# Optimization experiments

Measured on AMD Instinct MI355X. Metric: run time of the kernel, lower is better.

The kernel has to match this reference:

```python
import jax, jax.numpy as jnp
import numpy as np

N_NODES = 100000

def setup_inputs() -> dict:
    key = jax.random.key(0)
    k1, k2, k3 = jax.random.split(key, 3)
    x = jax.random.normal(k1, (N_NODES, 64), dtype=jnp.float32)
    edge_index = jax.random.randint(k2, (2, 1250000), 0, N_NODES, dtype=jnp.int64)
    edge_weight = jax.random.uniform(k3, (1250000,), dtype=jnp.float32)
    return {"x": x, "edge_index": edge_index, "edge_weight": edge_weight}

def reference(x, edge_index, edge_weight):
    # LightGCNConv: out[dst] = sum_e edge_weight[e] * x[src_e]  (aggr='add')
    src, dst = edge_index[0], edge_index[1]
    msgs = edge_weight[:, None] * x[src]          # [E, d] gather-multiply
    out = jax.ops.segment_sum(msgs, dst, num_segments=N_NODES)  # scatter-add
    return out
```

## Files before the change

kernel.cpp:

```cpp
#include <hip/hip_runtime.h>
#include <hip/hip_bf16.h>


#define N_NODES   100000
#define N_FEAT    64

#define A_BSH     7
#define A_NPB     (1 << A_BSH)
#define A_KB      ((N_NODES + A_NPB - 1) >> A_BSH)
#define A_CAP     2048
#define A_FCHUNK  8192
#define A_OVCAP   65536

__global__ __launch_bounds__(256) void k_cast(
    const float* __restrict__ x, ushort* __restrict__ xb) {
    int i = (blockIdx.x * 256 + threadIdx.x) * 4;
    if (i >= N_NODES * N_FEAT) return;
    float4 v = *(const float4*)(x + i);
    uint4 u = *(uint4*)&v;
    ushort4 r;
    r.x = (ushort)((u.x + 0x7FFFu + ((u.x >> 16) & 1)) >> 16);
    r.y = (ushort)((u.y + 0x7FFFu + ((u.y >> 16) & 1)) >> 16);
    r.z = (ushort)((u.z + 0x7FFFu + ((u.z >> 16) & 1)) >> 16);
    r.w = (ushort)((u.w + 0x7FFFu + ((u.w >> 16) & 1)) >> 16);
    *(ushort4*)(xb + i) = r;
}

__global__ __launch_bounds__(1024) void k_bin(
    const int* __restrict__ ei, const float* __restrict__ w,
    int* __restrict__ bcur, int2* __restrict__ stg,
    int* __restrict__ ovf, int* __restrict__ ovcnt, int E) {
    __shared__ int h[A_KB];
    int t = threadIdx.x;
    for (int b = t; b < A_KB; b += 1024) h[b] = 0;
    __syncthreads();
    int e0 = blockIdx.x * A_FCHUNK;
    #pragma unroll
    for (int k = 0; k < A_FCHUNK / 1024; ++k) {
        int e = e0 + k * 1024 + t;
        if (e < E) atomicAdd(&h[ei[E + e] >> A_BSH], 1);
    }
    __syncthreads();
    for (int b = t; b < A_KB; b += 1024) {
        int c = h[b];
        h[b] = c ? atomicAdd(&bcur[b], c) : 0;
    }
    __syncthreads();
    #pragma unroll
    for (int k = 0; k < A_FCHUNK / 1024; ++k) {
        int e = e0 + k * 1024 + t;
        if (e < E) {
            int dst = ei[E + e];
            int b = dst >> A_BSH;
            int loc = atomicAdd(&h[b], 1);
            if (loc < A_CAP) {
                stg[b * A_CAP + loc] =
                    make_int2(ei[e] | ((dst & (A_NPB - 1)) << 17),
                              __float_as_int(w[e]));
            } else {
                int oi = atomicAdd(ovcnt, 1);
                if (oi < A_OVCAP) ovf[oi] = e;
            }
        }
    }
}

__global__ __launch_bounds__(256) void k_sort(
    int2* __restrict__ stg, const int* __restrict__ bcur,
    int* __restrict__ beg, int* __restrict__ endp) {
    __shared__ int2 buf[A_CAP];
    __shared__ int  hist[A_NPB];
    __shared__ int  cur[A_NPB];
    __shared__ int  sdata[256];
    int b = blockIdx.x, t = threadIdx.x;
    int cnt = bcur[b];
    if (cnt > A_CAP) cnt = A_CAP;
    int base = b * A_CAP;

    if (t < A_NPB) hist[t] = 0;
    __syncthreads();
    for (int i = t; i < cnt; i += 256) {
        int2 p = stg[base + i];
        buf[i] = p;
        atomicAdd(&hist[(p.x >> 17) & (A_NPB - 1)], 1);
    }
    __syncthreads();
    int c = (t < A_NPB) ? hist[t] : 0;
    sdata[t] = c; __syncthreads();
    for (int off = 1; off < 256; off <<= 1) {
        int v = (t >= off) ? sdata[t - off] : 0;
        __syncthreads();
        if (t >= off) sdata[t] += v;
        __syncthreads();
    }
    int excl = (t == 0) ? 0 : sdata[t - 1];
    if (t < A_NPB) {
        cur[t] = excl;
        int node = (b << A_BSH) + t;
        if (node < N_NODES) { beg[node] = base + excl; endp[node] = base + excl + c; }
    }
    __syncthreads();
    for (int i = t; i < cnt; i += 256) {
        int2 p = buf[i];
        int pos = atomicAdd(&cur[(p.x >> 17) & (A_NPB - 1)], 1);
        stg[base + pos] = p;
    }
}

__global__ __launch_bounds__(256) void k_gather2(
    const ushort* __restrict__ xb, const int* __restrict__ beg,
    const int* __restrict__ endp, const int2* __restrict__ stg,
    float* __restrict__ out) {
    int wid  = threadIdx.x >> 6;
    int lane = threadIdx.x & 63;
    int half = lane >> 5;
    int l    = lane & 31;
    int node = blockIdx.x * 8 + wid * 2 + half;
    if (node >= N_NODES) return;
    int j = beg[node], end = endp[node];
    const ushort2* xb2 = (const ushort2*)xb;
    float a0x = 0.f, a0y = 0.f, a1x = 0.f, a1y = 0.f;
    for (; j + 3 < end; j += 4) {
        int2 p0 = stg[j];
        int2 p1 = stg[j + 1];
        int2 p2 = stg[j + 2];
        int2 p3 = stg[j + 3];
        ushort2 u0 = xb2[(size_t)(p0.x & 0x1FFFF) * 32 + l];
        ushort2 u1 = xb2[(size_t)(p1.x & 0x1FFFF) * 32 + l];
        ushort2 u2 = xb2[(size_t)(p2.x & 0x1FFFF) * 32 + l];
        ushort2 u3 = xb2[(size_t)(p3.x & 0x1FFFF) * 32 + l];
        float w0 = __int_as_float(p0.y), w1 = __int_as_float(p1.y);
        float w2 = __int_as_float(p2.y), w3 = __int_as_float(p3.y);
        a0x += w0 * __uint_as_float((uint)u0.x << 16);
        a0y += w0 * __uint_as_float((uint)u0.y << 16);
        a1x += w1 * __uint_as_float((uint)u1.x << 16);
        a1y += w1 * __uint_as_float((uint)u1.y << 16);
        a0x += w2 * __uint_as_float((uint)u2.x << 16);
        a0y += w2 * __uint_as_float((uint)u2.y << 16);
        a1x += w3 * __uint_as_float((uint)u3.x << 16);
        a1y += w3 * __uint_as_float((uint)u3.y << 16);
    }
    for (; j < end; ++j) {
        int2 p = stg[j];
        ushort2 u = xb2[(size_t)(p.x & 0x1FFFF) * 32 + l];
        float wv = __int_as_float(p.y);
        a0x += wv * __uint_as_float((uint)u.x << 16);
        a0y += wv * __uint_as_float((uint)u.y << 16);
    }
    float2 r; r.x = a0x + a1x; r.y = a0y + a1y;
    ((float2*)out)[(size_t)node * 32 + l] = r;
}

__global__ __launch_bounds__(256) void k_ovf(
    const float* __restrict__ x, const int* __restrict__ ei,
    const float* __restrict__ w, const int* __restrict__ ovf,
    const int* __restrict__ ovcnt, float* __restrict__ out, int E) {
    int n = *ovcnt;
    if (n > A_OVCAP) n = A_OVCAP;
    int wid  = blockIdx.x * 4 + (threadIdx.x >> 6);
    int lane = threadIdx.x & 63;
    for (int i = wid; i < n; i += gridDim.x * 4) {
        int e = ovf[i];
        float v = w[e] * x[(size_t)ei[e] * N_FEAT + lane];
        atomicAdd(&out[(size_t)ei[E + e] * N_FEAT + lane], v);
    }
}

#define BSH       8
#define NPB       (1 << BSH)
#define KB        ((N_NODES + NPB - 1) >> BSH)
#define FCHUNK    8192
#define SORT_CAP  4096

__global__ __launch_bounds__(256) void k_chist(
    const int* __restrict__ ei, int* __restrict__ bcur, int E) {
    __shared__ int h[KB];
    int t = threadIdx.x;
    for (int b = t; b < KB; b += 256) h[b] = 0;
    __syncthreads();
    int e0 = blockIdx.x * FCHUNK;
    #pragma unroll
    for (int k = 0; k < FCHUNK / 256; ++k) {
        int e = e0 + k * 256 + t;
        if (e < E) atomicAdd(&h[ei[E + e] >> BSH], 1);
    }
    __syncthreads();
    for (int b = t; b < KB; b += 256) if (h[b]) atomicAdd(&bcur[b], h[b]);
}

__global__ __launch_bounds__(256) void k_cscan(
    int* __restrict__ bcur, int* __restrict__ boffs) {
    __shared__ int sdata[256];
    int t = threadIdx.x;
    int i0 = 2 * t, i1 = 2 * t + 1;
    int v0 = (i0 < KB) ? bcur[i0] : 0;
    int v1 = (i1 < KB) ? bcur[i1] : 0;
    sdata[t] = v0 + v1; __syncthreads();
    for (int off = 1; off < 256; off <<= 1) {
        int v = (t >= off) ? sdata[t - off] : 0;
        __syncthreads();
        if (t >= off) sdata[t] += v;
        __syncthreads();
    }
    int run = (t == 0) ? 0 : sdata[t - 1];
    if (i0 < KB) { boffs[i0] = run; bcur[i0] = run; }
    run += v0;
    if (i1 < KB) { boffs[i1] = run; bcur[i1] = run; }
    if (t == 255) boffs[KB] = sdata[255];
}

__global__ __launch_bounds__(256) void k_cbin(
    const int* __restrict__ ei, const float* __restrict__ w,
    int* __restrict__ bcur, int2* __restrict__ stg, int E) {
    __shared__ int h[KB];
    int t = threadIdx.x;
    for (int b = t; b < KB; b += 256) h[b] = 0;
    __syncthreads();
    int e0 = blockIdx.x * FCHUNK;
    #pragma unroll
    for (int k = 0; k < FCHUNK / 256; ++k) {
        int e = e0 + k * 256 + t;
        if (e < E) atomicAdd(&h[ei[E + e] >> BSH], 1);
    }
    __syncthreads();
    for (int b = t; b < KB; b += 256) {
        int c = h[b];
        h[b] = c ? atomicAdd(&bcur[b], c) : 0;
    }
    __syncthreads();
    #pragma unroll
    for (int k = 0; k < FCHUNK / 256; ++k) {
        int e = e0 + k * 256 + t;
        if (e < E) {
            int dst = ei[E + e];
            int slot = atomicAdd(&h[dst >> BSH], 1);
            stg[slot] = make_int2(ei[e] | ((dst & (NPB - 1)) << 17),
                                  __float_as_int(w[e]));
        }
    }
}

__global__ __launch_bounds__(256) void k_csort(
    int2* __restrict__ stg, const int* __restrict__ boffs,
    int* __restrict__ offs) {
    __shared__ int2 buf[SORT_CAP];
    __shared__ int  hist[NPB];
    __shared__ int  cur[NPB];
    __shared__ int  sdata[256];
    int b = blockIdx.x, t = threadIdx.x;
    int bg = boffs[b], end = boffs[b + 1], cnt = end - bg;
    for (int n = t; n < NPB; n += 256) hist[n] = 0;
    __syncthreads();
    int nlds = cnt < SORT_CAP ? cnt : SORT_CAP;
    for (int i = t; i < nlds; i += 256) {
        int2 p = stg[bg + i];
        buf[i] = p;
        atomicAdd(&hist[(p.x >> 17) & (NPB - 1)], 1);
    }
    int2 r0{0,0}, r1{0,0}; int nr = 0;
    {
        int i0 = nlds + t, i1 = nlds + 256 + t;
        if (i0 < cnt) { r0 = stg[bg + i0]; atomicAdd(&hist[(r0.x >> 17) & (NPB - 1)], 1); nr = 1; }
        if (i1 < cnt) { r1 = stg[bg + i1]; atomicAdd(&hist[(r1.x >> 17) & (NPB - 1)], 1); nr = 2; }
    }
    __syncthreads();
    int c = hist[t];
    sdata[t] = c; __syncthreads();
    for (int off = 1; off < 256; off <<= 1) {
        int v = (t >= off) ? sdata[t - off] : 0;
        __syncthreads();
        if (t >= off) sdata[t] += v;
        __syncthreads();
    }
    int excl = (t == 0) ? 0 : sdata[t - 1];
    cur[t] = excl;
    int node = (b << BSH) + t;
    if (node < N_NODES) offs[node] = bg + excl;
    if (b == KB - 1 && t == 255) offs[N_NODES] = end;
    __syncthreads();
    for (int i = t; i < nlds; i += 256) {
        int2 p = buf[i];
        int pos = atomicAdd(&cur[(p.x >> 17) & (NPB - 1)], 1);
        stg[bg + pos] = p;
    }
    if (nr >= 1) { int pos = atomicAdd(&cur[(r0.x >> 17) & (NPB - 1)], 1); stg[bg + pos] = r0; }
    if (nr >= 2) { int pos = atomicAdd(&cur[(r1.x >> 17) & (NPB - 1)], 1); stg[bg + pos] = r1; }
}

__global__ __launch_bounds__(256) void k_gather(
    const float* __restrict__ x, const int* __restrict__ offs,
    const int2* __restrict__ stg, float* __restrict__ out) {
    int node = blockIdx.x * 4 + (threadIdx.x >> 6);
    int lane = threadIdx.x & 63;
    if (node >= N_NODES) return;
    int bg = offs[node], end = offs[node + 1];
    float a0 = 0.f, a1 = 0.f, a2 = 0.f, a3 = 0.f;
    int j = bg;
    for (; j + 3 < end; j += 4) {
        int2 p0 = stg[j];
        int2 p1 = stg[j + 1];
        int2 p2 = stg[j + 2];
        int2 p3 = stg[j + 3];
        a0 += __int_as_float(p0.y) * x[(size_t)(p0.x & 0x1FFFF) * N_FEAT + lane];
        a1 += __int_as_float(p1.y) * x[(size_t)(p1.x & 0x1FFFF) * N_FEAT + lane];
        a2 += __int_as_float(p2.y) * x[(size_t)(p2.x & 0x1FFFF) * N_FEAT + lane];
        a3 += __int_as_float(p3.y) * x[(size_t)(p3.x & 0x1FFFF) * N_FEAT + lane];
    }
    for (; j < end; ++j) {
        int2 p = stg[j];
        a0 += __int_as_float(p.y) * x[(size_t)(p.x & 0x1FFFF) * N_FEAT + lane];
    }
    out[(size_t)node * N_FEAT + lane] = (a0 + a1) + (a2 + a3);
}

__global__ __launch_bounds__(256) void gnn_scatter_kernel(
    const float* __restrict__ x, const int* __restrict__ ei,
    const float* __restrict__ w, float* __restrict__ out, int E) {
    int e = blockIdx.x * 4 + (threadIdx.x >> 6);
    int lane = threadIdx.x & 63;
    if (e >= E) return;
    float v = w[e] * x[(size_t)ei[e] * N_FEAT + lane];
    atomicAdd(&out[(size_t)ei[E + e] * N_FEAT + lane], v);
}

static inline size_t align16(size_t v) { return (v + 15) & ~(size_t)15; }

extern "C" void kernel_launch(void* const* d_in, const int* in_sizes, int n_in,
                              void* d_out, int out_size, void* d_ws, size_t ws_size,
                              hipStream_t stream) {
    const float* x   = (const float*)d_in[0];
    const int*   ei  = (const int*)d_in[1];
    const float* w   = (const float*)d_in[2];
    float*       out = (float*)d_out;
    const int E = in_sizes[2];
    char* ws = (char*)d_ws;

    size_t a_xb   = 0;
    size_t a_stg  = align16(a_xb + (size_t)N_NODES * N_FEAT * 2);
    size_t a_beg  = align16(a_stg + (size_t)A_KB * A_CAP * 8);
    size_t a_end  = align16(a_beg + (size_t)N_NODES * 4);
    size_t a_bcur = align16(a_end + (size_t)N_NODES * 4);
    size_t a_ovf  = align16(a_bcur + (size_t)(A_KB + 1) * 4);
    size_t need_a = a_ovf + (size_t)A_OVCAP * 4;

    if (ws_size >= need_a) {
        ushort* xb   = (ushort*)(ws + a_xb);
        int2*   stg  = (int2*)(ws + a_stg);
        int*    beg  = (int*)(ws + a_beg);
        int*    endp = (int*)(ws + a_end);
        int*    bcur = (int*)(ws + a_bcur);
        int*    ovcnt = bcur + A_KB;
        int*    ovf  = (int*)(ws + a_ovf);

        hipMemsetAsync(bcur, 0, (size_t)(A_KB + 1) * 4, stream);
        k_cast<<<(N_NODES * N_FEAT / 4 + 255) / 256, 256, 0, stream>>>(x, xb);
        k_bin<<<(E + A_FCHUNK - 1) / A_FCHUNK, 1024, 0, stream>>>(
            ei, w, bcur, stg, ovf, ovcnt, E);
        k_sort<<<A_KB, 256, 0, stream>>>(stg, bcur, beg, endp);
        k_gather2<<<(N_NODES + 7) / 8, 256, 0, stream>>>(xb, beg, endp, stg, out);
        k_ovf<<<16, 256, 0, stream>>>(x, ei, w, ovf, ovcnt, out, E);
        return;
    }

    size_t b_bcur  = 0;
    size_t b_boffs = align16(b_bcur + (size_t)KB * 4);
    size_t b_offs  = align16(b_boffs + (size_t)(KB + 1) * 4);
    size_t b_stg   = align16(b_offs + (size_t)(N_NODES + 1) * 4);
    size_t need_b  = b_stg + (size_t)E * 8;

    if (ws_size >= need_b) {
        int*  bcur  = (int*)(ws + b_bcur);
        int*  boffs = (int*)(ws + b_boffs);
        int*  offs  = (int*)(ws + b_offs);
        int2* stg   = (int2*)(ws + b_stg);
        const int nblk = (E + FCHUNK - 1) / FCHUNK;
        hipMemsetAsync(bcur, 0, (size_t)KB * 4, stream);
        k_chist<<<nblk, 256, 0, stream>>>(ei, bcur, E);
        k_cscan<<<1, 256, 0, stream>>>(bcur, boffs);
        k_cbin<<<nblk, 256, 0, stream>>>(ei, w, bcur, stg, E);
        k_csort<<<KB, 256, 0, stream>>>(stg, boffs, offs);
        k_gather<<<(N_NODES + 3) / 4, 256, 0, stream>>>(x, offs, stg, out);
        return;
    }

    hipMemsetAsync(d_out, 0, (size_t)out_size * sizeof(float), stream);
    gnn_scatter_kernel<<<(E + 3) / 4, 256, 0, stream>>>(x, ei, w, out, E);
}
```

Baseline: 158.7 us.

## Fuse bf16 cast into binning kernel and widen gather to 16 lanes per node

The separate cast kernel is folded into the binning kernel as extra blocks, so the fp32-to-bf16 conversion runs concurrently with edge binning in one launch. The gather kernel now handles each node with 16 lanes loading ushort4 (8 bytes) instead of 32 lanes loading ushort2, and writes float4 results, processing 16 nodes per block. The goal is to save a launch, overlap independent work, and issue wider memory accesses in the gather. The fast path is now additionally gated on E matching the fixed edge count, because the launch grid size is hardcoded.

```diff
diff --git a/kernel.cpp b/kernel.cpp
--- a/kernel.cpp
+++ b/kernel.cpp
@@ -11,27 +11,34 @@
 #define A_CAP     2048
 #define A_FCHUNK  8192
 #define A_OVCAP   65536
-
-__global__ __launch_bounds__(256) void k_cast(
-    const float* __restrict__ x, ushort* __restrict__ xb) {
-    int i = (blockIdx.x * 256 + threadIdx.x) * 4;
-    if (i >= N_NODES * N_FEAT) return;
-    float4 v = *(const float4*)(x + i);
-    uint4 u = *(uint4*)&v;
-    ushort4 r;
-    r.x = (ushort)((u.x + 0x7FFFu + ((u.x >> 16) & 1)) >> 16);
-    r.y = (ushort)((u.y + 0x7FFFu + ((u.y >> 16) & 1)) >> 16);
-    r.z = (ushort)((u.z + 0x7FFFu + ((u.z >> 16) & 1)) >> 16);
-    r.w = (ushort)((u.w + 0x7FFFu + ((u.w >> 16) & 1)) >> 16);
-    *(ushort4*)(xb + i) = r;
-}
-
-__global__ __launch_bounds__(1024) void k_bin(
+#define NBIN      ((1250000 + A_FCHUNK - 1) / A_FCHUNK)
+#define NCAST     391
+
+__global__ __launch_bounds__(1024) void k_castbin(
+    const float* __restrict__ x, ushort* __restrict__ xb,
     const int* __restrict__ ei, const float* __restrict__ w,
     int* __restrict__ bcur, int2* __restrict__ stg,
     int* __restrict__ ovf, int* __restrict__ ovcnt, int E) {
+    int t = threadIdx.x;
+    if (blockIdx.x >= NBIN) {
+        int cb = blockIdx.x - NBIN;
+        #pragma unroll
+        for (int k = 0; k < 4; ++k) {
+            int i4 = cb * 4096 + k * 1024 + t;
+            if (i4 < N_NODES * N_FEAT / 4) {
+                float4 v = ((const float4*)x)[i4];
+                uint4 u = *(uint4*)&v;
+                ushort4 r;
+                r.x = (ushort)((u.x + 0x7FFFu + ((u.x >> 16) & 1)) >> 16);
+                r.y = (ushort)((u.y + 0x7FFFu + ((u.y >> 16) & 1)) >> 16);
+                r.z = (ushort)((u.z + 0x7FFFu + ((u.z >> 16) & 1)) >> 16);
+                r.w = (ushort)((u.w + 0x7FFFu + ((u.w >> 16) & 1)) >> 16);
+                ((ushort4*)xb)[i4] = r;
+            }
+        }
+        return;
+    }
     __shared__ int h[A_KB];
-    int t = threadIdx.x;
     for (int b = t; b < A_KB; b += 1024) h[b] = 0;
     __syncthreads();
     int e0 = blockIdx.x * A_FCHUNK;
@@ -107,48 +114,47 @@
     }
 }
 
-__global__ __launch_bounds__(256) void k_gather2(
+__global__ __launch_bounds__(256) void k_gather4(
     const ushort* __restrict__ xb, const int* __restrict__ beg,
     const int* __restrict__ endp, const int2* __restrict__ stg,
     float* __restrict__ out) {
     int wid  = threadIdx.x >> 6;
     int lane = threadIdx.x & 63;
-    int half = lane >> 5;
-    int l    = lane & 31;
-    int node = blockIdx.x * 8 + wid * 2 + half;
+    int q    = lane >> 4;
+    int l    = lane & 15;
+    int node = blockIdx.x * 16 + wid * 4 + q;
     if (node >= N_NODES) return;
     int j = beg[node], end = endp[node];
-    const ushort2* xb2 = (const ushort2*)xb;
-    float a0x = 0.f, a0y = 0.f, a1x = 0.f, a1y = 0.f;
-    for (; j + 3 < end; j += 4) {
+    const ushort4* xb4 = (const ushort4*)xb;
+    float ax0 = 0.f, ay0 = 0.f, az0 = 0.f, aw0 = 0.f;
+    float ax1 = 0.f, ay1 = 0.f, az1 = 0.f, aw1 = 0.f;
+    for (; j + 1 < end; j += 2) {
         int2 p0 = stg[j];
         int2 p1 = stg[j + 1];
-        int2 p2 = stg[j + 2];
-        int2 p3 = stg[j + 3];
-        ushort2 u0 = xb2[(size_t)(p0.x & 0x1FFFF) * 32 + l];
-        ushort2 u1 = xb2[(size_t)(p1.x & 0x1FFFF) * 32 + l];
-        ushort2 u2 = xb2[(size_t)(p2.x & 0x1FFFF) * 32 + l];
-        ushort2 u3 = xb2[(size_t)(p3.x & 0x1FFFF) * 32 + l];
+        ushort4 u0 = xb4[(size_t)(p0.x & 0x1FFFF) * 16 + l];
+        ushort4 u1 = xb4[(size_t)(p1.x & 0x1FFFF) * 16 + l];
         float w0 = __int_as_float(p0.y), w1 = __int_as_float(p1.y);
-        float w2 = __int_as_float(p2.y), w3 = __int_as_float(p3.y);
-        a0x += w0 * __uint_as_float((uint)u0.x << 16);
-        a0y += w0 * __uint_as_float((uint)u0.y << 16);
-        a1x += w1 * __uint_as_float((uint)u1.x << 16);
-        a1y += w1 * __uint_as_float((uint)u1.y << 16);
-        a0x += w2 * __uint_as_float((uint)u2.x << 16);
-        a0y += w2 * __uint_as_float((uint)u2.y << 16);
-        a1x += w3 * __uint_as_float((uint)u3.x << 16);
-        a1y += w3 * __uint_as_float((uint)u3.y << 16);
-    }
-    for (; j < end; ++j) {
+        ax0 += w0 * __uint_as_float((uint)u0.x << 16);
+        ay0 += w0 * __uint_as_float((uint)u0.y << 16);
+        az0 += w0 * __uint_as_float((uint)u0.z << 16);
+        aw0 += w0 * __uint_as_float((uint)u0.w << 16);
+        ax1 += w1 * __uint_as_float((uint)u1.x << 16);
+        ay1 += w1 * __uint_as_float((uint)u1.y << 16);
+        az1 += w1 * __uint_as_float((uint)u1.z << 16);
+        aw1 += w1 * __uint_as_float((uint)u1.w << 16);
+    }
+    if (j < end) {
         int2 p = stg[j];
-        ushort2 u = xb2[(size_t)(p.x & 0x1FFFF) * 32 + l];
+        ushort4 u = xb4[(size_t)(p.x & 0x1FFFF) * 16 + l];
         float wv = __int_as_float(p.y);
-        a0x += wv * __uint_as_float((uint)u.x << 16);
-        a0y += wv * __uint_as_float((uint)u.y << 16);
-    }
-    float2 r; r.x = a0x + a1x; r.y = a0y + a1y;
-    ((float2*)out)[(size_t)node * 32 + l] = r;
+        ax0 += wv * __uint_as_float((uint)u.x << 16);
+        ay0 += wv * __uint_as_float((uint)u.y << 16);
+        az0 += wv * __uint_as_float((uint)u.z << 16);
+        aw0 += wv * __uint_as_float((uint)u.w << 16);
+    }
+    float4 r;
+    r.x = ax0 + ax1; r.y = ay0 + ay1; r.z = az0 + az1; r.w = aw0 + aw1;
+    ((float4*)out)[(size_t)node * 16 + l] = r;
 }
 
 __global__ __launch_bounds__(256) void k_ovf(
@@ -343,7 +349,7 @@
     size_t a_ovf  = align16(a_bcur + (size_t)(A_KB + 1) * 4);
     size_t need_a = a_ovf + (size_t)A_OVCAP * 4;
 
-    if (ws_size >= need_a) {
+    if (ws_size >= need_a && E == 1250000) {
         ushort* xb   = (ushort*)(ws + a_xb);
         int2*   stg  = (int2*)(ws + a_stg);
         int*    beg  = (int*)(ws + a_beg);
@@ -353,11 +359,10 @@
         int*    ovf  = (int*)(ws + a_ovf);
 
         hipMemsetAsync(bcur, 0, (size_t)(A_KB + 1) * 4, stream);
-        k_cast<<<(N_NODES * N_FEAT / 4 + 255) / 256, 256, 0, stream>>>(x, xb);
-        k_bin<<<(E + A_FCHUNK - 1) / A_FCHUNK, 1024, 0, stream>>>(
-            ei, w, bcur, stg, ovf, ovcnt, E);
+        k_castbin<<<NBIN + NCAST, 1024, 0, stream>>>(
+            x, xb, ei, w, bcur, stg, ovf, ovcnt, E);
         k_sort<<<A_KB, 256, 0, stream>>>(stg, bcur, beg, endp);
-        k_gather2<<<(N_NODES + 7) / 8, 256, 0, stream>>>(xb, beg, endp, stg, out);
+        k_gather4<<<(N_NODES + 15) / 16, 256, 0, stream>>>(xb, beg, endp, stg, out);
         k_ovf<<<16, 256, 0, stream>>>(x, ei, w, ovf, ovcnt, out, E);
         return;
     }
```

Result: no change. 158.4 us (-0.2%).
